# Optimization experiments

Hardware: AMD Instinct MI355X
Metric: run time of the kernel (lower is better)

The kernel has to match this reference:

```python
import jax, jax.numpy as jnp
import numpy as np

D_MODEL = 1024
NUM_EXPERTS = 8
TOP_K = 2


def setup_inputs() -> dict:
    key = jax.random.key(0)
    ks = jax.random.split(key, 8)
    d, e = D_MODEL, NUM_EXPERTS
    s = 0.02
    return {
        "x": jax.random.normal(ks[0], (2, 2048, d), dtype=jnp.float32),
        "router_w": jax.random.normal(ks[1], (d, e), dtype=jnp.float32) * s,
        "router_b": jnp.zeros((e,), dtype=jnp.float32),
        "w1": jax.random.normal(ks[2], (e, d, 4 * d), dtype=jnp.float32) * s,
        "b1": jnp.zeros((e, 4 * d), dtype=jnp.float32),
        "w2": jax.random.normal(ks[3], (e, 4 * d, d), dtype=jnp.float32) * s,
        "b2": jnp.zeros((e, d), dtype=jnp.float32),
    }


def reference(x, router_w, router_b, w1, b1, w2, b2):
    orig_shape = x.shape
    d = x.shape[-1]
    xf = x.reshape(-1, d)                      # [T, d]
    T = xf.shape[0]

    logits = xf @ router_w + router_b          # [T, E]
    probs = jax.nn.softmax(logits, axis=-1)    # [T, E]
    top_v, top_i = jax.lax.top_k(probs, TOP_K)  # [T, k]
    top_v = top_v / jnp.sum(top_v, axis=-1, keepdims=True)

    # dense combine weights, zero except the top-k experts per token
    comb = jnp.zeros_like(probs).at[jnp.arange(T)[:, None], top_i].add(top_v)  # [T, E]

    # run every expert on every token (dense grouped GEMM), then weighted combine
    h = jax.nn.gelu(jnp.einsum("td,edf->etf", xf, w1) + b1[:, None, :], approximate=False)  # [E, T, 4d]
    y = jnp.einsum("etf,efd->etd", h, w2) + b2[:, None, :]                                   # [E, T, d]
    out = jnp.einsum("te,etd->td", comb, y)                                                   # [T, d]

    mean_probs = probs.mean(axis=0)
    aux_loss = jnp.var(mean_probs, ddof=1)     # torch.var default is unbiased
    return out.reshape(orig_shape), aux_loss
```

## Files before the change

kernel.cpp:

```cpp
#include <hip/hip_runtime.h>


#define TOKENS 4096
#define DMODEL 1024
#define NEXP   8
#define DFF    4096
#define NROWS  (2*TOKENS)
#define SPLITK 2

typedef __bf16 bf16_t;
typedef __bf16 bf16x8 __attribute__((ext_vector_type(8)));
typedef __bf16 bf16x4 __attribute__((ext_vector_type(4)));
typedef float  f32x4  __attribute__((ext_vector_type(4)));

__device__ __forceinline__ void gl_lds16(const void* g, void* l) {
    __builtin_amdgcn_global_load_lds(
        (const __attribute__((address_space(1))) void*)g,
        (__attribute__((address_space(3))) void*)l, 16, 0, 0);
}

__global__ __launch_bounds__(256) void router_k(
    const float* __restrict__ x, const float* __restrict__ rw,
    const float* __restrict__ rb, int* __restrict__ cnt,
    int* __restrict__ tok_e, int* __restrict__ tok_pos,
    float* __restrict__ tok_w, float* __restrict__ probs,
    bf16_t* __restrict__ xb)
{
    int w = threadIdx.x >> 6;
    int lane = threadIdx.x & 63;
    int t = blockIdx.x * 4 + w;
    const float* xr = x + (size_t)t * DMODEL;
    bf16_t* xbr = xb + (size_t)t * DMODEL;
    float s[NEXP];
#pragma unroll
    for (int e = 0; e < NEXP; e++) s[e] = 0.f;
#pragma unroll
    for (int i4 = 0; i4 < 4; i4++) {
        int i = (i4 * 64 + lane) * 4;
        float4 v = *(const float4*)(xr + i);
        bf16x4 b;
        b[0] = (bf16_t)v.x; b[1] = (bf16_t)v.y; b[2] = (bf16_t)v.z; b[3] = (bf16_t)v.w;
        *(bf16x4*)(xbr + i) = b;
        const float* wr = rw + (size_t)i * NEXP;
#pragma unroll
        for (int e = 0; e < NEXP; e++)
            s[e] += v.x * wr[e] + v.y * wr[NEXP + e] + v.z * wr[2 * NEXP + e]
                  + v.w * wr[3 * NEXP + e];
    }
#pragma unroll
    for (int e = 0; e < NEXP; e++) {
#pragma unroll
        for (int o = 32; o > 0; o >>= 1) s[e] += __shfl_down(s[e], o, 64);
    }
    if (lane == 0) {
        float mx = -1e30f;
#pragma unroll
        for (int e = 0; e < NEXP; e++) { s[e] += rb[e]; mx = fmaxf(mx, s[e]); }
        float den = 0.f;
#pragma unroll
        for (int e = 0; e < NEXP; e++) { s[e] = expf(s[e] - mx); den += s[e]; }
        float inv = 1.f / den;
#pragma unroll
        for (int e = 0; e < NEXP; e++) { s[e] *= inv; probs[t * NEXP + e] = s[e]; }
        int e0 = 0;
#pragma unroll
        for (int e = 1; e < NEXP; e++) if (s[e] > s[e0]) e0 = e;
        int e1 = (e0 == 0) ? 1 : 0;
#pragma unroll
        for (int e = 0; e < NEXP; e++) if (e != e0 && s[e] > s[e1]) e1 = e;
        float sw = s[e0] + s[e1];
        int p0 = atomicAdd(&cnt[e0], 1);
        int p1 = atomicAdd(&cnt[e1], 1);
        tok_e[2 * t] = e0;       tok_e[2 * t + 1] = e1;
        tok_pos[2 * t] = p0;     tok_pos[2 * t + 1] = p1;
        tok_w[2 * t] = s[e0] / sw; tok_w[2 * t + 1] = s[e1] / sw;
    }
}

__global__ void offsets_k(const int* __restrict__ cnt, int* __restrict__ off)
{
    if (threadIdx.x == 0) {
        int a = 0;
        for (int e = 0; e < NEXP; e++) { off[e] = a; a += cnt[e]; }
        off[NEXP] = a;
    }
}

__global__ void scatter_k(const int* __restrict__ tok_e, const int* __restrict__ tok_pos,
                          const float* __restrict__ tok_w, const int* __restrict__ off,
                          int* __restrict__ rows_tok, float* __restrict__ roww,
                          int* __restrict__ g_of)
{
    int i = blockIdx.x * blockDim.x + threadIdx.x;
    if (i < 2 * TOKENS) {
        int e = tok_e[i];
        int g = off[e] + tok_pos[i];
        rows_tok[g] = i >> 1;
        roww[g] = tok_w[i];
        g_of[i] = g;
    }
}

#define TP2 65
__global__ __launch_bounds__(256) void transconv_k(const float* __restrict__ in,
                                                   bf16_t* __restrict__ o, int K, int N)
{
    __shared__ float t[128 * TP2];
    int e = blockIdx.z;
    int n0 = blockIdx.x * 64, k0 = blockIdx.y * 128;
    int tid = threadIdx.x;
    int c4 = (tid & 15) * 4, r = tid >> 4;
    const float* src = in + ((size_t)e * K + k0) * N + n0;
#pragma unroll
    for (int p = 0; p < 8; p++) {
        int k = r + p * 16;
        float4 v = *(const float4*)(src + (size_t)k * N + c4);
        float* d = &t[k * TP2 + c4];
        d[0] = v.x; d[1] = v.y; d[2] = v.z; d[3] = v.w;
    }
    __syncthreads();
    int k8 = tid & 15, n = tid >> 4;
    bf16_t* dst = o + ((size_t)e * N + n0) * K + k0;
#pragma unroll
    for (int p = 0; p < 4; p++) {
        int nn = n + p * 16;
        bf16x8 w;
#pragma unroll
        for (int j = 0; j < 8; j++) w[j] = (bf16_t)t[(k8 * 8 + j) * TP2 + nn];
        *(bf16x8*)(dst + (size_t)nn * K + k8 * 8) = w;
    }
}

__global__ __launch_bounds__(256, 2) void gemm1_k(
    const bf16_t* __restrict__ A, const bf16_t* __restrict__ Bt,
    const float* __restrict__ bias,
    const int* __restrict__ cnt, const int* __restrict__ off,
    const int* __restrict__ rows_tok, bf16_t* __restrict__ hbuf)
{
    int bid = blockIdx.x;
    int e = bid & 7;
    int rest = bid >> 3;
    int yt = rest & 31;
    int xt = rest >> 5;
    int M = cnt[e];
    int m0 = yt * 128;
    if (m0 >= M) return;
    int n0 = xt * 128;
    int base = off[e];

    __shared__ __align__(16) bf16_t lA[128 * 64];
    __shared__ __align__(16) bf16_t lB[128 * 64];

    int tid = threadIdx.x;
    int wave = tid >> 6;
    int lane = tid & 63;
    int sc = (lane & 7) ^ (lane >> 3);

    const bf16_t* aRow[4];
    const bf16_t* bRow[4];
#pragma unroll
    for (int i = 0; i < 4; i++) {
        int r = (wave * 4 + i) * 8 + (lane >> 3);
        int gr = m0 + r; if (gr > M - 1) gr = M - 1;
        int tok = rows_tok[base + gr];
        aRow[i] = A + (size_t)tok * DMODEL;
        bRow[i] = Bt + ((size_t)e * DFF + n0 + r) * DMODEL;
    }

    f32x4 acc[4][4];
    f32x4 zero = { 0.f, 0.f, 0.f, 0.f };
#pragma unroll
    for (int i = 0; i < 4; i++)
#pragma unroll
        for (int j = 0; j < 4; j++) acc[i][j] = zero;

    int wrow = wave >> 1, wcol = wave & 1;

#pragma unroll 1
    for (int kk = 0; kk < DMODEL / 64; ++kk) {
        int koff = kk * 64 + sc * 8;
#pragma unroll
        for (int i = 0; i < 4; i++) {
            gl_lds16(aRow[i] + koff, &lA[(wave * 4 + i) * 512]);
            gl_lds16(bRow[i] + koff, &lB[(wave * 4 + i) * 512]);
        }
        __syncthreads();
#pragma unroll
        for (int ks = 0; ks < 2; ++ks) {
            bf16x8 af[4], bfr[4];
#pragma unroll
            for (int mt = 0; mt < 4; mt++) {
                int r = wrow * 64 + mt * 16 + (lane & 15);
                int ch = (ks * 4 + (lane >> 4)) ^ (r & 7);
                af[mt] = *(const bf16x8*)&lA[r * 64 + ch * 8];
            }
#pragma unroll
            for (int nt = 0; nt < 4; nt++) {
                int c = wcol * 64 + nt * 16 + (lane & 15);
                int ch = (ks * 4 + (lane >> 4)) ^ (c & 7);
                bfr[nt] = *(const bf16x8*)&lB[c * 64 + ch * 8];
            }
#pragma unroll
            for (int mt = 0; mt < 4; mt++)
#pragma unroll
                for (int nt = 0; nt < 4; nt++)
                    acc[mt][nt] = __builtin_amdgcn_mfma_f32_16x16x32_bf16(
                        af[mt], bfr[nt], acc[mt][nt], 0, 0, 0);
        }
        __syncthreads();
    }

    float bv[4];
#pragma unroll
    for (int nt = 0; nt < 4; nt++)
        bv[nt] = bias[(size_t)e * DFF + n0 + wcol * 64 + nt * 16 + (lane & 15)];

#pragma unroll
    for (int mt = 0; mt < 4; mt++) {
#pragma unroll
        for (int q = 0; q < 4; q++) {
            int r = wrow * 64 + mt * 16 + (lane >> 4) * 4 + q;
            int gm = m0 + r;
            if (gm < M) {
                size_t hrow = (size_t)(base + gm) * DFF;
#pragma unroll
                for (int nt = 0; nt < 4; nt++) {
                    float v = acc[mt][nt][q] + bv[nt];
                    v = 0.5f * v * (1.f + erff(v * 0.70710678118654752f));
                    int c = n0 + wcol * 64 + nt * 16 + (lane & 15);
                    hbuf[hrow + c] = (bf16_t)v;
                }
            }
        }
    }
}

__global__ __launch_bounds__(256, 2) void gemm2_k(
    const bf16_t* __restrict__ A, const bf16_t* __restrict__ Bt,
    const int* __restrict__ cnt, const int* __restrict__ off,
    bf16_t* __restrict__ ybuf)
{
    int bid = blockIdx.x;
    int e = bid & 7;
    int rest = bid >> 3;
    int yt = rest & 31;
    int xt = (rest >> 5) & 7;
    int kt = rest >> 8;
    int M = cnt[e];
    int m0 = yt * 128;
    if (m0 >= M) return;
    int n0 = xt * 128;
    int base = off[e];
    int k0 = kt * (DFF / SPLITK);

    __shared__ __align__(16) bf16_t lA[128 * 64];
    __shared__ __align__(16) bf16_t lB[128 * 64];

    int tid = threadIdx.x;
    int wave = tid >> 6;
    int lane = tid & 63;
    int sc = (lane & 7) ^ (lane >> 3);

    const bf16_t* aRow[4];
    const bf16_t* bRow[4];
#pragma unroll
    for (int i = 0; i < 4; i++) {
        int r = (wave * 4 + i) * 8 + (lane >> 3);
        int gr = m0 + r; if (gr > M - 1) gr = M - 1;
        aRow[i] = A + (size_t)(base + gr) * DFF + k0;
        bRow[i] = Bt + ((size_t)e * DMODEL + n0 + r) * DFF + k0;
    }

    f32x4 acc[4][4];
    f32x4 zero = { 0.f, 0.f, 0.f, 0.f };
#pragma unroll
    for (int i = 0; i < 4; i++)
#pragma unroll
        for (int j = 0; j < 4; j++) acc[i][j] = zero;

    int wrow = wave >> 1, wcol = wave & 1;

#pragma unroll 1
    for (int kk = 0; kk < (DFF / SPLITK) / 64; ++kk) {
        int koff = kk * 64 + sc * 8;
#pragma unroll
        for (int i = 0; i < 4; i++) {
            gl_lds16(aRow[i] + koff, &lA[(wave * 4 + i) * 512]);
            gl_lds16(bRow[i] + koff, &lB[(wave * 4 + i) * 512]);
        }
        __syncthreads();
#pragma unroll
        for (int ks = 0; ks < 2; ++ks) {
            bf16x8 af[4], bfr[4];
#pragma unroll
            for (int mt = 0; mt < 4; mt++) {
                int r = wrow * 64 + mt * 16 + (lane & 15);
                int ch = (ks * 4 + (lane >> 4)) ^ (r & 7);
                af[mt] = *(const bf16x8*)&lA[r * 64 + ch * 8];
            }
#pragma unroll
            for (int nt = 0; nt < 4; nt++) {
                int c = wcol * 64 + nt * 16 + (lane & 15);
                int ch = (ks * 4 + (lane >> 4)) ^ (c & 7);
                bfr[nt] = *(const bf16x8*)&lB[c * 64 + ch * 8];
            }
#pragma unroll
            for (int mt = 0; mt < 4; mt++)
#pragma unroll
                for (int nt = 0; nt < 4; nt++)
                    acc[mt][nt] = __builtin_amdgcn_mfma_f32_16x16x32_bf16(
                        af[mt], bfr[nt], acc[mt][nt], 0, 0, 0);
        }
        __syncthreads();
    }

#pragma unroll
    for (int mt = 0; mt < 4; mt++) {
#pragma unroll
        for (int q = 0; q < 4; q++) {
            int r = wrow * 64 + mt * 16 + (lane >> 4) * 4 + q;
            int gm = m0 + r;
            if (gm < M) {
                size_t yrow = ((size_t)kt * NROWS + base + gm) * DMODEL;
#pragma unroll
                for (int nt = 0; nt < 4; nt++) {
                    int c = n0 + wcol * 64 + nt * 16 + (lane & 15);
                    ybuf[yrow + c] = (bf16_t)acc[mt][nt][q];
                }
            }
        }
    }
}

__global__ __launch_bounds__(256) void combine_k(
    const bf16_t* __restrict__ ybuf, const int* __restrict__ g_of,
    const int* __restrict__ tok_e, const float* __restrict__ tok_w,
    const float* __restrict__ b2, float* __restrict__ out)
{
    int t = blockIdx.x;
    int c = threadIdx.x * 4;
    int g0 = g_of[2 * t], g1 = g_of[2 * t + 1];
    int e0 = tok_e[2 * t], e1 = tok_e[2 * t + 1];
    float w0 = tok_w[2 * t], w1 = tok_w[2 * t + 1];
    float a0[4] = {0.f, 0.f, 0.f, 0.f}, a1[4] = {0.f, 0.f, 0.f, 0.f};
#pragma unroll
    for (int kt = 0; kt < SPLITK; kt++) {
        bf16x4 y0 = *(const bf16x4*)&ybuf[((size_t)kt * NROWS + g0) * DMODEL + c];
        bf16x4 y1 = *(const bf16x4*)&ybuf[((size_t)kt * NROWS + g1) * DMODEL + c];
#pragma unroll
        for (int j = 0; j < 4; j++) { a0[j] += (float)y0[j]; a1[j] += (float)y1[j]; }
    }
    float4 bb0 = *(const float4*)&b2[(size_t)e0 * DMODEL + c];
    float4 bb1 = *(const float4*)&b2[(size_t)e1 * DMODEL + c];
    float4 r;
    r.x = w0 * (a0[0] + bb0.x) + w1 * (a1[0] + bb1.x);
    r.y = w0 * (a0[1] + bb0.y) + w1 * (a1[1] + bb1.y);
    r.z = w0 * (a0[2] + bb0.z) + w1 * (a1[2] + bb1.z);
    r.w = w0 * (a0[3] + bb0.w) + w1 * (a1[3] + bb1.w);
    *(float4*)&out[(size_t)t * DMODEL + c] = r;
}

__global__ __launch_bounds__(256) void aux1_k(const float* __restrict__ probs,
                                              float* __restrict__ partial)
{
    int t = blockIdx.x * 256 + threadIdx.x;
    const float4* pr = (const float4*)(probs + (size_t)t * NEXP);
    float4 a = pr[0], b = pr[1];
    float v[8] = { a.x, a.y, a.z, a.w, b.x, b.y, b.z, b.w };
#pragma unroll
    for (int e = 0; e < 8; e++)
#pragma unroll
        for (int o = 32; o > 0; o >>= 1) v[e] += __shfl_down(v[e], o, 64);
    __shared__ float sm[4][8];
    int wave = threadIdx.x >> 6, lane = threadIdx.x & 63;
    if (lane == 0)
#pragma unroll
        for (int e = 0; e < 8; e++) sm[wave][e] = v[e];
    __syncthreads();
    if (threadIdx.x < 8) {
        float s = sm[0][threadIdx.x] + sm[1][threadIdx.x]
                + sm[2][threadIdx.x] + sm[3][threadIdx.x];
        partial[blockIdx.x * 8 + threadIdx.x] = s;
    }
}

__global__ __launch_bounds__(128) void aux2_k(const float* __restrict__ partial,
                                              float* __restrict__ out_aux)
{
    __shared__ float sm[16][8];
    __shared__ float me[8];
    int tid = threadIdx.x;
    sm[tid >> 3][tid & 7] = partial[tid];
    __syncthreads();
    if (tid < 8) {
        float s = 0.f;
        for (int g = 0; g < 16; g++) s += sm[g][tid];
        me[tid] = s / (float)TOKENS;
    }
    __syncthreads();
    if (tid == 0) {
        float mean = 0.f;
        for (int e = 0; e < 8; e++) mean += me[e];
        mean /= 8.f;
        float v = 0.f;
        for (int e = 0; e < 8; e++) { float d = me[e] - mean; v += d * d; }
        out_aux[0] = v / 7.f;
    }
}

extern "C" void kernel_launch(void* const* d_in, const int* in_sizes, int n_in,
                              void* d_out, int out_size, void* d_ws, size_t ws_size,
                              hipStream_t stream)
{
    const float* x  = (const float*)d_in[0];
    const float* rw = (const float*)d_in[1];
    const float* rb = (const float*)d_in[2];
    const float* w1 = (const float*)d_in[3];
    const float* b1 = (const float*)d_in[4];
    const float* w2 = (const float*)d_in[5];
    const float* b2 = (const float*)d_in[6];
    float* out = (float*)d_out;

    char* p = (char*)d_ws;
    auto alloc = [&](size_t b) { char* q = p; p += (b + 255) & ~(size_t)255; return q; };
    int*    cnt      = (int*)   alloc(NEXP * sizeof(int));
    int*    off      = (int*)   alloc((NEXP + 1) * sizeof(int));
    int*    tok_e    = (int*)   alloc(2 * TOKENS * sizeof(int));
    int*    tok_pos  = (int*)   alloc(2 * TOKENS * sizeof(int));
    float*  tok_w    = (float*) alloc(2 * TOKENS * sizeof(float));
    int*    rows_tok = (int*)   alloc(NROWS * sizeof(int));
    float*  roww     = (float*) alloc(NROWS * sizeof(float));
    int*    g_of     = (int*)   alloc(2 * TOKENS * sizeof(int));
    float*  probs    = (float*) alloc((size_t)TOKENS * NEXP * sizeof(float));
    float*  aux_part = (float*) alloc(16 * NEXP * sizeof(float));
    bf16_t* xb       = (bf16_t*)alloc((size_t)TOKENS * DMODEL * 2);
    bf16_t* w1t      = (bf16_t*)alloc((size_t)NEXP * DFF * DMODEL * 2);
    bf16_t* w2t      = (bf16_t*)alloc((size_t)NEXP * DMODEL * DFF * 2);
    bf16_t* hbuf     = (bf16_t*)alloc((size_t)NROWS * DFF * 2);
    bf16_t* ybuf     = w1t;

    hipMemsetAsync(cnt, 0, NEXP * sizeof(int), stream);

    router_k<<<TOKENS / 4, 256, 0, stream>>>(x, rw, rb, cnt, tok_e, tok_pos, tok_w, probs, xb);
    offsets_k<<<1, 64, 0, stream>>>(cnt, off);
    scatter_k<<<(2 * TOKENS + 255) / 256, 256, 0, stream>>>(tok_e, tok_pos, tok_w, off,
                                                            rows_tok, roww, g_of);
    transconv_k<<<dim3(DFF / 64, DMODEL / 128, NEXP), 256, 0, stream>>>(w1, w1t, DMODEL, DFF);
    transconv_k<<<dim3(DMODEL / 64, DFF / 128, NEXP), 256, 0, stream>>>(w2, w2t, DFF, DMODEL);

    gemm1_k<<<NEXP * 32 * 32, 256, 0, stream>>>(xb, w1t, b1, cnt, off, rows_tok, hbuf);
    gemm2_k<<<NEXP * 32 * 8 * SPLITK, 256, 0, stream>>>(hbuf, w2t, cnt, off, ybuf);
    combine_k<<<TOKENS, 256, 0, stream>>>(ybuf, g_of, tok_e, tok_w, b2, out);

    aux1_k<<<TOKENS / 256, 256, 0, stream>>>(probs, aux_part);
    aux2_k<<<1, 128, 0, stream>>>(aux_part, out + (size_t)TOKENS * DMODEL);
}
```

Measured before the change: 647.8 us.

## Fuse weight transposes into router and gemm1 kernels to overlap independent work

Merges the w1 transpose-convert into the router kernel and the w2 transpose-convert into gemm1 by interleaving block roles, so independent weight preprocessing overlaps with routing and the first GEMM. Offsets and scatter are merged into a single one-block kernel, and the aux reduction is folded into combine. This cuts launch count and fills the GPU during otherwise serialized phases. In exchange, the combined kernels use the larger shared memory footprint for every block, and the scatter now runs on a single block.

```diff
diff --git a/kernel.cpp b/kernel.cpp
--- a/kernel.cpp
+++ b/kernel.cpp
@@ -7,6 +7,7 @@
 #define DFF    4096
 #define NROWS  (2*TOKENS)
 #define SPLITK 2
+#define TP2    65
 
 typedef __bf16 bf16_t;
 typedef __bf16 bf16x8 __attribute__((ext_vector_type(8)));
@@ -19,16 +20,55 @@
         (__attribute__((address_space(3))) void*)l, 16, 0, 0);
 }
 
-__global__ __launch_bounds__(256) void router_k(
+__device__ __forceinline__ void transconv_dev(const float* __restrict__ in,
+                                              bf16_t* __restrict__ o, int K, int N,
+                                              int xg, int yg, int e, float* t, int tid)
+{
+    int n0 = xg * 64, k0 = yg * 128;
+    int c4 = (tid & 15) * 4, r = tid >> 4;
+    const float* src = in + ((size_t)e * K + k0) * N + n0;
+#pragma unroll
+    for (int p = 0; p < 8; p++) {
+        int k = r + p * 16;
+        float4 v = *(const float4*)(src + (size_t)k * N + c4);
+        float* d = &t[k * TP2 + c4];
+        d[0] = v.x; d[1] = v.y; d[2] = v.z; d[3] = v.w;
+    }
+    __syncthreads();
+    int k8 = tid & 15, n = tid >> 4;
+    bf16_t* dst = o + ((size_t)e * N + n0) * K + k0;
+#pragma unroll
+    for (int p = 0; p < 4; p++) {
+        int nn = n + p * 16;
+        bf16x8 w;
+#pragma unroll
+        for (int j = 0; j < 8; j++) w[j] = (bf16_t)t[(k8 * 8 + j) * TP2 + nn];
+        *(bf16x8*)(dst + (size_t)nn * K + k8 * 8) = w;
+    }
+}
+
+__global__ __launch_bounds__(256) void router_tw1_k(
     const float* __restrict__ x, const float* __restrict__ rw,
     const float* __restrict__ rb, int* __restrict__ cnt,
     int* __restrict__ tok_e, int* __restrict__ tok_pos,
     float* __restrict__ tok_w, float* __restrict__ probs,
-    bf16_t* __restrict__ xb)
-{
-    int w = threadIdx.x >> 6;
-    int lane = threadIdx.x & 63;
-    int t = blockIdx.x * 4 + w;
+    bf16_t* __restrict__ xb,
+    const float* __restrict__ w1, bf16_t* __restrict__ w1t)
+{
+    __shared__ __align__(16) char smem[128 * TP2 * 4];
+    int P = blockIdx.x % 5, C = blockIdx.x / 5;
+    int tid = threadIdx.x;
+    if (P < 4) {
+        int idx = C * 4 + P;
+        int xg = idx & 63;
+        int yg = (idx >> 6) & 7;
+        int eg = idx >> 9;
+        transconv_dev(w1, w1t, DMODEL, DFF, xg, yg, eg, (float*)smem, tid);
+        return;
+    }
+    int w = tid >> 6;
+    int lane = tid & 63;
+    int t = C * 4 + w;
     const float* xr = x + (size_t)t * DMODEL;
     bf16_t* xbr = xb + (size_t)t * DMODEL;
     float s[NEXP];
@@ -77,81 +117,59 @@
     }
 }
 
-__global__ void offsets_k(const int* __restrict__ cnt, int* __restrict__ off)
-{
+__global__ __launch_bounds__(256) void offsets_scatter_k(
+    const int* __restrict__ cnt, int* __restrict__ off,
+    const int* __restrict__ tok_e, const int* __restrict__ tok_pos,
+    const float* __restrict__ tok_w,
+    int* __restrict__ rows_tok, float* __restrict__ roww, int* __restrict__ g_of)
+{
+    __shared__ int soff[NEXP];
     if (threadIdx.x == 0) {
         int a = 0;
-        for (int e = 0; e < NEXP; e++) { off[e] = a; a += cnt[e]; }
+        for (int e = 0; e < NEXP; e++) { soff[e] = a; off[e] = a; a += cnt[e]; }
         off[NEXP] = a;
     }
-}
-
-__global__ void scatter_k(const int* __restrict__ tok_e, const int* __restrict__ tok_pos,
-                          const float* __restrict__ tok_w, const int* __restrict__ off,
-                          int* __restrict__ rows_tok, float* __restrict__ roww,
-                          int* __restrict__ g_of)
-{
-    int i = blockIdx.x * blockDim.x + threadIdx.x;
-    if (i < 2 * TOKENS) {
+    __syncthreads();
+    for (int i = threadIdx.x; i < 2 * TOKENS; i += 256) {
         int e = tok_e[i];
-        int g = off[e] + tok_pos[i];
+        int g = soff[e] + tok_pos[i];
         rows_tok[g] = i >> 1;
         roww[g] = tok_w[i];
         g_of[i] = g;
     }
 }
 
-#define TP2 65
-__global__ __launch_bounds__(256) void transconv_k(const float* __restrict__ in,
-                                                   bf16_t* __restrict__ o, int K, int N)
-{
-    __shared__ float t[128 * TP2];
-    int e = blockIdx.z;
-    int n0 = blockIdx.x * 64, k0 = blockIdx.y * 128;
-    int tid = threadIdx.x;
-    int c4 = (tid & 15) * 4, r = tid >> 4;
-    const float* src = in + ((size_t)e * K + k0) * N + n0;
-#pragma unroll
-    for (int p = 0; p < 8; p++) {
-        int k = r + p * 16;
-        float4 v = *(const float4*)(src + (size_t)k * N + c4);
-        float* d = &t[k * TP2 + c4];
-        d[0] = v.x; d[1] = v.y; d[2] = v.z; d[3] = v.w;
-    }
-    __syncthreads();
-    int k8 = tid & 15, n = tid >> 4;
-    bf16_t* dst = o + ((size_t)e * N + n0) * K + k0;
-#pragma unroll
-    for (int p = 0; p < 4; p++) {
-        int nn = n + p * 16;
-        bf16x8 w;
-#pragma unroll
-        for (int j = 0; j < 8; j++) w[j] = (bf16_t)t[(k8 * 8 + j) * TP2 + nn];
-        *(bf16x8*)(dst + (size_t)nn * K + k8 * 8) = w;
-    }
-}
-
-__global__ __launch_bounds__(256, 2) void gemm1_k(
+__global__ __launch_bounds__(256, 2) void gemm1_tw2_k(
     const bf16_t* __restrict__ A, const bf16_t* __restrict__ Bt,
     const float* __restrict__ bias,
     const int* __restrict__ cnt, const int* __restrict__ off,
-    const int* __restrict__ rows_tok, bf16_t* __restrict__ hbuf)
-{
-    int bid = blockIdx.x;
-    int e = bid & 7;
-    int rest = bid >> 3;
-    int yt = rest & 31;
-    int xt = rest >> 5;
+    const int* __restrict__ rows_tok, bf16_t* __restrict__ hbuf,
+    const float* __restrict__ w2, bf16_t* __restrict__ w2t)
+{
+    __shared__ __align__(16) char smem[128 * TP2 * 4];
+    int P = blockIdx.x % 24, C = blockIdx.x / 24;
+    int tid = threadIdx.x;
+    if (P >= 16) {
+        int idx = C * 8 + (P - 16);
+        int xg = idx & 15;
+        int yg = (idx >> 4) & 31;
+        int eg = idx >> 9;
+        transconv_dev(w2, w2t, DFF, DMODEL, xg, yg, eg, (float*)smem, tid);
+        return;
+    }
+    int e = P & 7;
+    int local = C * 2 + (P >> 3);
+    int yt = local & 31;
+    int xt = local >> 5;
     int M = cnt[e];
     int m0 = yt * 128;
     if (m0 >= M) return;
     int n0 = xt * 128;
     int base = off[e];
 
-    __shared__ __align__(16) bf16_t lA[128 * 64];
-    __shared__ __align__(16) bf16_t lB[128 * 64];
-
-    int tid = threadIdx.x;
+    bf16_t* lA = (bf16_t*)smem;
+    bf16_t* lB = lA + 128 * 64;
+
     int wave = tid >> 6;
     int lane = tid & 63;
     int sc = (lane & 7) ^ (lane >> 3);
@@ -332,11 +350,35 @@
     }
 }
 
-__global__ __launch_bounds__(256) void combine_k(
+__global__ __launch_bounds__(256) void combine_aux1_k(
     const bf16_t* __restrict__ ybuf, const int* __restrict__ g_of,
     const int* __restrict__ tok_e, const float* __restrict__ tok_w,
-    const float* __restrict__ b2, float* __restrict__ out)
-{
+    const float* __restrict__ b2, float* __restrict__ out,
+    const float* __restrict__ probs, float* __restrict__ partial)
+{
+    __shared__ float sm[4][8];
+    if (blockIdx.x >= TOKENS) {
+        int blk = blockIdx.x - TOKENS;
+        int t = blk * 256 + threadIdx.x;
+        const float4* pr = (const float4*)(probs + (size_t)t * NEXP);
+        float4 a = pr[0], b = pr[1];
+        float v[8] = { a.x, a.y, a.z, a.w, b.x, b.y, b.z, b.w };
+#pragma unroll
+        for (int e = 0; e < 8; e++)
+#pragma unroll
+            for (int o = 32; o > 0; o >>= 1) v[e] += __shfl_down(v[e], o, 64);
+        int wave = threadIdx.x >> 6, lane = threadIdx.x & 63;
+        if (lane == 0)
+#pragma unroll
+            for (int e = 0; e < 8; e++) sm[wave][e] = v[e];
+        __syncthreads();
+        if (threadIdx.x < 8) {
+            float s = sm[0][threadIdx.x] + sm[1][threadIdx.x]
+                    + sm[2][threadIdx.x] + sm[3][threadIdx.x];
+            partial[blk * 8 + threadIdx.x] = s;
+        }
+        return;
+    }
     int t = blockIdx.x;
     int c = threadIdx.x * 4;
     int g0 = g_of[2 * t], g1 = g_of[2 * t + 1];
@@ -358,30 +400,6 @@
     r.z = w0 * (a0[2] + bb0.z) + w1 * (a1[2] + bb1.z);
     r.w = w0 * (a0[3] + bb0.w) + w1 * (a1[3] + bb1.w);
     *(float4*)&out[(size_t)t * DMODEL + c] = r;
-}
-
-__global__ __launch_bounds__(256) void aux1_k(const float* __restrict__ probs,
-                                              float* __restrict__ partial)
-{
-    int t = blockIdx.x * 256 + threadIdx.x;
-    const float4* pr = (const float4*)(probs + (size_t)t * NEXP);
-    float4 a = pr[0], b = pr[1];
-    float v[8] = { a.x, a.y, a.z, a.w, b.x, b.y, b.z, b.w };
-#pragma unroll
-    for (int e = 0; e < 8; e++)
-#pragma unroll
-        for (int o = 32; o > 0; o >>= 1) v[e] += __shfl_down(v[e], o, 64);
-    __shared__ float sm[4][8];
-    int wave = threadIdx.x >> 6, lane = threadIdx.x & 63;
-    if (lane == 0)
-#pragma unroll
-        for (int e = 0; e < 8; e++) sm[wave][e] = v[e];
-    __syncthreads();
-    if (threadIdx.x < 8) {
-        float s = sm[0][threadIdx.x] + sm[1][threadIdx.x]
-                + sm[2][threadIdx.x] + sm[3][threadIdx.x];
-        partial[blockIdx.x * 8 + threadIdx.x] = s;
-    }
 }
 
 __global__ __launch_bounds__(128) void aux2_k(const float* __restrict__ partial,
@@ -441,17 +459,14 @@
 
     hipMemsetAsync(cnt, 0, NEXP * sizeof(int), stream);
 
-    router_k<<<TOKENS / 4, 256, 0, stream>>>(x, rw, rb, cnt, tok_e, tok_pos, tok_w, probs, xb);
-    offsets_k<<<1, 64, 0, stream>>>(cnt, off);
-    scatter_k<<<(2 * TOKENS + 255) / 256, 256, 0, stream>>>(tok_e, tok_pos, tok_w, off,
-                                                            rows_tok, roww, g_of);
-    transconv_k<<<dim3(DFF / 64, DMODEL / 128, NEXP), 256, 0, stream>>>(w1, w1t, DMODEL, DFF);
-    transconv_k<<<dim3(DMODEL / 64, DFF / 128, NEXP), 256, 0, stream>>>(w2, w2t, DFF, DMODEL);
-
-    gemm1_k<<<NEXP * 32 * 32, 256, 0, stream>>>(xb, w1t, b1, cnt, off, rows_tok, hbuf);
+    router_tw1_k<<<5120, 256, 0, stream>>>(x, rw, rb, cnt, tok_e, tok_pos, tok_w,
+                                           probs, xb, w1, w1t);
+    offsets_scatter_k<<<1, 256, 0, stream>>>(cnt, off, tok_e, tok_pos, tok_w,
+                                             rows_tok, roww, g_of);
+    gemm1_tw2_k<<<12288, 256, 0, stream>>>(xb, w1t, b1, cnt, off, rows_tok, hbuf,
+                                           w2, w2t);
     gemm2_k<<<NEXP * 32 * 8 * SPLITK, 256, 0, stream>>>(hbuf, w2t, cnt, off, ybuf);
-    combine_k<<<TOKENS, 256, 0, stream>>>(ybuf, g_of, tok_e, tok_w, b2, out);
-
-    aux1_k<<<TOKENS / 256, 256, 0, stream>>>(probs, aux_part);
+    combine_aux1_k<<<TOKENS + 16, 256, 0, stream>>>(ybuf, g_of, tok_e, tok_w, b2, out,
+                                                    probs, aux_part);
     aux2_k<<<1, 128, 0, stream>>>(aux_part, out + (size_t)TOKENS * DMODEL);
 }
```

Measured after the change: 578.2 us. 1.12x faster.
